# Optimization experiments

Measured on AMD Instinct MI355X. Metric: run time of the kernel, lower is better.

Reference implementation:

```python
import jax, jax.numpy as jnp
import numpy as np

N = 50000          # num graph nodes
E = 800000         # edges per direction
NGRAM, ODIM = 4, 32
DIMS = [128, 128, 64]
CLASSES = 128
MAXPE = 10
L2_EPS = 1e-12


def setup_inputs() -> dict:
    key = jax.random.key(0)
    ks = iter(jax.random.split(key, 40))
    d = {}
    d['x'] = jax.random.normal(next(ks), (N, DIMS[0]), jnp.float32)
    d['edge_index_in'] = jax.random.randint(next(ks), (2, E), 0, N, dtype=jnp.int64)
    d['edge_weight_in'] = jax.random.uniform(next(ks), (E,), jnp.float32)
    d['edge_index_out'] = jax.random.randint(next(ks), (2, E), 0, N, dtype=jnp.int64)
    d['edge_weight_out'] = jax.random.uniform(next(ks), (E,), jnp.float32)
    d['pe_table'] = jax.random.normal(next(ks), (MAXPE, ODIM), jnp.float32) * 0.05
    # per-layer DirectGCNLayer params (weights stored [in,out], i.e. torch W.T)
    for l in range(2):
        di, do = DIMS[l], DIMS[l + 1]
        s = 1.0 / np.sqrt(di)
        d[f'W_main_in_{l}'] = jax.random.normal(next(ks), (di, do), jnp.float32) * s
        d[f'W_main_out_{l}'] = jax.random.normal(next(ks), (di, do), jnp.float32) * s
        d[f'W_shared_{l}'] = jax.random.normal(next(ks), (di, do), jnp.float32) * s
        d[f'b_main_in_{l}'] = jnp.zeros((do,), jnp.float32)
        d[f'b_main_out_{l}'] = jnp.zeros((do,), jnp.float32)
        d[f'b_shared_in_{l}'] = jnp.zeros((do,), jnp.float32)
        d[f'b_shared_out_{l}'] = jnp.zeros((do,), jnp.float32)
        d[f'C_in_{l}'] = jnp.ones((N, 1), jnp.float32)
        d[f'C_out_{l}'] = jnp.ones((N, 1), jnp.float32)
    # residual projection for layer 1 (128 -> 64); layer 0 is identity
    d['res_W_1'] = jax.random.normal(next(ks), (DIMS[1], DIMS[2]), jnp.float32) * (1.0 / np.sqrt(DIMS[1]))
    d['res_b_1'] = jnp.zeros((DIMS[2],), jnp.float32)
    d['dec_W'] = jax.random.normal(next(ks), (DIMS[2], CLASSES), jnp.float32) * (1.0 / np.sqrt(DIMS[2]))
    d['dec_b'] = jnp.zeros((CLASSES,), jnp.float32)
    return d


def _prop(xW, ei, ew):
    # gather source, scale by edge weight, scatter-add to target (PyG aggr='add')
    return jax.ops.segment_sum(ew[:, None] * xW[ei[0]], ei[1], num_segments=N)


def _layer(h, ei_in, ew_in, ei_out, ew_out,
           Wmi, Wmo, Ws, bmi, bmo, bsi, bso, cin, cout):
    xs = h @ Ws  # shared transform, propagated over both edge sets
    ic = _prop(h @ Wmi, ei_in, ew_in) + bmi + _prop(xs, ei_in, ew_in) + bsi
    oc = _prop(h @ Wmo, ei_out, ew_out) + bmo + _prop(xs, ei_out, ew_out) + bso
    return cin * ic + cout * oc


def reference(x, edge_index_in, edge_weight_in, edge_index_out, edge_weight_out,
              pe_table,
              W_main_in_0, W_main_out_0, W_shared_0, b_main_in_0, b_main_out_0,
              b_shared_in_0, b_shared_out_0, C_in_0, C_out_0,
              W_main_in_1, W_main_out_1, W_shared_1, b_main_in_1, b_main_out_1,
              b_shared_in_1, b_shared_out_1, C_in_1, C_out_1,
              res_W_1, res_b_1, dec_W, dec_b):
    # positional encoding: add pe[:n_gram_len] to each n-gram slot
    h = (x.reshape(N, NGRAM, ODIM) + pe_table[:NGRAM][None]).reshape(N, NGRAM * ODIM)
    # layer 0 (identity residual); dropout p=0 / eval -> no-op
    h = jnp.tanh(_layer(h, edge_index_in, edge_weight_in, edge_index_out, edge_weight_out,
                        W_main_in_0, W_main_out_0, W_shared_0, b_main_in_0, b_main_out_0,
                        b_shared_in_0, b_shared_out_0, C_in_0, C_out_0) + h)
    # layer 1 (linear residual projection 128 -> 64)
    h = jnp.tanh(_layer(h, edge_index_in, edge_weight_in, edge_index_out, edge_weight_out,
                        W_main_in_1, W_main_out_1, W_shared_1, b_main_in_1, b_main_out_1,
                        b_shared_in_1, b_shared_out_1, C_in_1, C_out_1)
                 + h @ res_W_1 + res_b_1)
    logits = h @ dec_W + dec_b
    logp = jax.nn.log_softmax(logits, axis=-1)
    emb = h / (jnp.linalg.norm(h, axis=1, keepdims=True) + L2_EPS)
    return logp, emb
```

## Files before the change

### kernel.cpp

```cpp
#include <hip/hip_runtime.h>
#include <hip/hip_bf16.h>
#include <math.h>

typedef __hip_bfloat16  bf16;
typedef __hip_bfloat162 bf162;
typedef __attribute__((ext_vector_type(8))) short short8;
typedef __attribute__((ext_vector_type(4))) float floatx4;

#define BSZ     128
#define NBMAX   512
#define PACHUNK 8192

__device__ inline float4 bf4_to_f4(uint2 v) {
  float2 lo = __bfloat1622float2(*(bf162*)&v.x);
  float2 hi = __bfloat1622float2(*(bf162*)&v.y);
  return make_float4(lo.x, lo.y, hi.x, hi.y);
}
__device__ inline uint2 f4_to_bf4(float4 v) {
  bf162 lo = __float22bfloat162_rn(make_float2(v.x, v.y));
  bf162 hi = __float22bfloat162_rn(make_float2(v.z, v.w));
  uint2 r;
  r.x = *(unsigned*)&lo;
  r.y = *(unsigned*)&hi;
  return r;
}

__global__ __launch_bounds__(256) void k_bhist(const int* __restrict__ eiIn, const int* __restrict__ eiOut,
                                               int E, int* __restrict__ bcnt, int NB) {
  __shared__ int h[NBMAX];
  const int t = threadIdx.x;
  const int set = blockIdx.y;
  const int* dst = (set ? eiOut : eiIn) + E;
  for (int i = t; i < NB; i += 256) h[i] = 0;
  __syncthreads();
  const int base = blockIdx.x * PACHUNK;
  const int m = min(PACHUNK, E - base);
  #pragma unroll 4
  for (int r = 0; r < PACHUNK / 256; ++r) {
    int i = r * 256 + t;
    if (i < m) atomicAdd(&h[dst[base + i] >> 7], 1);
  }
  __syncthreads();
  for (int i = t; i < NB; i += 256) {
    int c = h[i];
    if (c) atomicAdd(&bcnt[set * NBMAX + i], c);
  }
}

__global__ __launch_bounds__(64) void k_bscan(const int* __restrict__ bcnt,
                                              int* __restrict__ BO, int* __restrict__ bcur, int NB) {
  const int set = blockIdx.x;
  const int t = threadIdx.x;
  int carry = 0;
  for (int base = 0; base < NB; base += 64) {
    int idx = base + t;
    int v = (idx < NB) ? bcnt[set * NBMAX + idx] : 0;
    int incl = v;
    #pragma unroll
    for (int d = 1; d < 64; d <<= 1) {
      int u = __shfl_up(incl, d, 64);
      if (t >= d) incl += u;
    }
    if (idx < NB) {
      int e = carry + incl - v;
      BO[set * NBMAX + idx]   = e;
      bcur[set * NBMAX + idx] = e;
    }
    carry += __shfl(incl, 63, 64);
  }
}

__global__ __launch_bounds__(256) void k_partA(const int* __restrict__ eiIn, const float* __restrict__ ewIn,
                                               const int* __restrict__ eiOut, const float* __restrict__ ewOut,
                                               int E, int* __restrict__ bucketCur,
                                               int2* __restrict__ sI, int2* __restrict__ sO, int NB) {
  __shared__ int2 staged[PACHUNK];
  __shared__ int cnt[NBMAX];
  __shared__ int sb[NBMAX];
  const int t = threadIdx.x;
  const int set = blockIdx.y;
  const int*   ei = set ? eiOut : eiIn;
  const float* ew = set ? ewOut : ewIn;
  int2* stg  = set ? sO : sI;
  int*  bcur = bucketCur + set * NBMAX;
  const int base = blockIdx.x * PACHUNK;
  const int m = min(PACHUNK, E - base);
  for (int b = t; b < NB; b += 256) cnt[b] = 0;
  __syncthreads();
  #pragma unroll 4
  for (int r = 0; r < PACHUNK / 256; ++r) {
    int i = r * 256 + t;
    if (i < m) atomicAdd(&cnt[ei[E + base + i] >> 7], 1);
  }
  __syncthreads();
  if (t < 64) {
    int carry = 0;
    int nch = (NB + 63) >> 6;
    for (int c = 0; c < nch; ++c) {
      int idx = c * 64 + t;
      int v = (idx < NB) ? cnt[idx] : 0;
      int incl = v;
      #pragma unroll
      for (int d = 1; d < 64; d <<= 1) {
        int u = __shfl_up(incl, d, 64);
        if (t >= d) incl += u;
      }
      if (idx < NB) sb[idx] = carry + incl - v;
      carry += __shfl(incl, 63, 64);
    }
  }
  __syncthreads();
  for (int b = t; b < NB; b += 256) {
    int c = cnt[b];
    if (c > 0) cnt[b] = atomicAdd(&bcur[b], c) - sb[b];
  }
  __syncthreads();
  #pragma unroll 4
  for (int r = 0; r < PACHUNK / 256; ++r) {
    int i = r * 256 + t;
    if (i < m) {
      int src = ei[base + i];
      int dst = ei[E + base + i];
      float w = ew[base + i];
      int b = dst >> 7;
      int rank = atomicAdd(&sb[b], 1);
      staged[rank] = make_int2(src | ((dst & 127) << 16) | (b << 23), __float_as_int(w));
    }
  }
  __syncthreads();
  #pragma unroll 4
  for (int r = 0; r < PACHUNK / 256; ++r) {
    int j = r * 256 + t;
    if (j < m) {
      int2 p = staged[j];
      int b = ((unsigned)p.x) >> 23;
      stg[cnt[b] + j] = p;
    }
  }
}

__global__ __launch_bounds__(256) void k_partB(const int* __restrict__ BO, const int* __restrict__ bcur,
                                               const int2* __restrict__ sI, const int2* __restrict__ sO,
                                               int2* __restrict__ eI, int2* __restrict__ eO,
                                               int* __restrict__ offsI, int* __restrict__ offsO, int N) {
  __shared__ int cnt[BSZ];
  __shared__ int excl[BSZ];
  __shared__ int cur[BSZ];
  const int t = threadIdx.x;
  const int b = blockIdx.x;
  const int set = blockIdx.y;
  const int2* stg = set ? sO : sI;
  int2* out = set ? eO : eI;
  int*  offs = set ? offsO : offsI;
  const int nlo = b << 7;
  const int nodes = min(BSZ, N - nlo);
  const int lo = BO[set * NBMAX + b];
  const int hi = bcur[set * NBMAX + b];
  if (t < BSZ) cnt[t] = 0;
  __syncthreads();
  for (int i = lo + t; i < hi; i += 256) atomicAdd(&cnt[(stg[i].x >> 16) & 127], 1);
  __syncthreads();
  if (t < 64) {
    int v0 = cnt[t];
    int i0 = v0;
    #pragma unroll
    for (int d = 1; d < 64; d <<= 1) { int u = __shfl_up(i0, d, 64); if (t >= d) i0 += u; }
    int v1 = cnt[64 + t];
    int i1 = v1;
    #pragma unroll
    for (int d = 1; d < 64; d <<= 1) { int u = __shfl_up(i1, d, 64); if (t >= d) i1 += u; }
    int tot0 = __shfl(i0, 63, 64);
    excl[t]      = i0 - v0;
    excl[64 + t] = tot0 + i1 - v1;
  }
  __syncthreads();
  if (t < BSZ) cur[t] = lo + excl[t];
  if (t < nodes) offs[nlo + t] = lo + excl[t];
  if (b == gridDim.x - 1 && t == 0) offs[N] = hi;
  __syncthreads();
  for (int i = lo + t; i < hi; i += 256) {
    int2 p = stg[i];
    int dl = (p.x >> 16) & 127;
    int pos = atomicAdd(&cur[dl], 1);
    out[pos] = make_int2(p.x & 0xffff, p.y);
  }
}

__global__ void k_wprep(const float* __restrict__ Wmi0, const float* __restrict__ Wmo0, const float* __restrict__ Ws0,
                        const float* __restrict__ Wmi1, const float* __restrict__ Wmo1, const float* __restrict__ Ws1,
                        const float* __restrict__ resW,
                        const float* __restrict__ bmi0, const float* __restrict__ bsi0,
                        const float* __restrict__ bmo0, const float* __restrict__ bso0,
                        const float* __restrict__ bmi1, const float* __restrict__ bsi1,
                        const float* __restrict__ bmo1, const float* __restrict__ bso1,
                        float* __restrict__ Wstack0, float* __restrict__ Wcat1,
                        float* __restrict__ bi0, float* __restrict__ bo0,
                        float* __restrict__ bi1, float* __restrict__ bo1) {
  int i = blockIdx.x * blockDim.x + threadIdx.x;
  if (i < 128 * 128) {
    Wstack0[i]             = Wmi0[i] + Ws0[i];
    Wstack0[128 * 128 + i] = Wmo0[i] + Ws0[i];
  }
  if (i < 128 * 192) {
    int k = i / 192, n = i % 192;
    float v;
    if (n < 64)       v = Wmi1[k * 64 + n]       + Ws1[k * 64 + n];
    else if (n < 128) v = Wmo1[k * 64 + n - 64]  + Ws1[k * 64 + n - 64];
    else              v = resW[k * 64 + n - 128];
    Wcat1[k * 192 + n] = v;
  }
  if (i < 128) { bi0[i] = bmi0[i] + bsi0[i]; bo0[i] = bmo0[i] + bso0[i]; }
  if (i < 64)  { bi1[i] = bmi1[i] + bsi1[i]; bo1[i] = bmo1[i] + bso1[i]; }
}

__device__ inline void pack_one(const float* __restrict__ W, bf16* __restrict__ P,
                                int id, int NT, int DO) {
  int lane = id & 63;
  int tile = id >> 6;
  int nt = tile % NT, kt = tile / NT;
  int col  = nt * 16 + (lane & 15);
  int krow = kt * 32 + (lane >> 4) * 8;
  bf16* dst = P + (size_t)id * 8;
  #pragma unroll
  for (int j = 0; j < 8; ++j) dst[j] = __float2bfloat16(W[(size_t)(krow + j) * DO + col]);
}
__global__ void k_packall(const float* __restrict__ W0, const float* __restrict__ W1,
                          const float* __restrict__ Wd,
                          bf16* __restrict__ P0, bf16* __restrict__ P1, bf16* __restrict__ Pd) {
  int id = blockIdx.x * blockDim.x + threadIdx.x;
  const int T0 = 8 * 8 * 64;
  const int T1 = 4 * 12 * 64;
  const int Td = 2 * 8 * 64;
  if (id < T0)                pack_one(W0, P0, id, 8, 128);
  else if (id < T0 + T1)      pack_one(W1, P1, id - T0, 12, 192);
  else if (id < T0 + T1 + Td) pack_one(Wd, Pd, id - T0 - T1, 8, 128);
}

__global__ void k_prep0(const float* __restrict__ x, const float* __restrict__ pe,
                        bf16* __restrict__ h0, int total) {
  int i = blockIdx.x * blockDim.x + threadIdx.x;
  if (i < total) h0[i] = __float2bfloat16(x[i] + pe[i & 127]);
}

__global__ __launch_bounds__(256) void k_agg0(const bf16* __restrict__ tb,
                                              const int* __restrict__ offsI, const int2* __restrict__ eI,
                                              const int* __restrict__ offsO, const int2* __restrict__ eO,
                                              const float* __restrict__ cin, const float* __restrict__ cou,
                                              bf16* __restrict__ aggC, int N) {
  int n = (blockIdx.x * blockDim.x + threadIdx.x) >> 6;
  int lane = threadIdx.x & 63;
  if (n >= N) return;
  const int dir = lane >> 5;
  const int sub = (lane >> 4) & 1;
  const int sl  = lane & 15;
  const int*   offs = dir ? offsO : offsI;
  const int2*  el   = dir ? eO : eI;
  const float* cc   = dir ? cou : cin;
  const char* base = (const char*)tb + sl * 16;
  float a0 = 0, a1 = 0, a2 = 0, a3 = 0, a4 = 0, a5 = 0, a6 = 0, a7 = 0;
  const int s0 = offs[n], s1 = offs[n + 1];
  int i = s0 + sub;
  for (; i + 6 < s1; i += 8) {
    int2 eA = el[i], eB = el[i + 2], eC = el[i + 4], eD = el[i + 6];
    uint4 vA = *(const uint4*)(base + ((size_t)(unsigned)eA.x << 8));
    uint4 vB = *(const uint4*)(base + ((size_t)(unsigned)eB.x << 8));
    uint4 vC = *(const uint4*)(base + ((size_t)(unsigned)eC.x << 8));
    uint4 vD = *(const uint4*)(base + ((size_t)(unsigned)eD.x << 8));
    float wA = __int_as_float(eA.y), wB = __int_as_float(eB.y);
    float wC = __int_as_float(eC.y), wD = __int_as_float(eD.y);
    float4 Al = bf4_to_f4(make_uint2(vA.x, vA.y)), Ah = bf4_to_f4(make_uint2(vA.z, vA.w));
    float4 Bl = bf4_to_f4(make_uint2(vB.x, vB.y)), Bh = bf4_to_f4(make_uint2(vB.z, vB.w));
    float4 Cl = bf4_to_f4(make_uint2(vC.x, vC.y)), Ch = bf4_to_f4(make_uint2(vC.z, vC.w));
    float4 Dl = bf4_to_f4(make_uint2(vD.x, vD.y)), Dh = bf4_to_f4(make_uint2(vD.z, vD.w));
    a0 += wA * Al.x + wB * Bl.x + wC * Cl.x + wD * Dl.x;
    a1 += wA * Al.y + wB * Bl.y + wC * Cl.y + wD * Dl.y;
    a2 += wA * Al.z + wB * Bl.z + wC * Cl.z + wD * Dl.z;
    a3 += wA * Al.w + wB * Bl.w + wC * Cl.w + wD * Dl.w;
    a4 += wA * Ah.x + wB * Bh.x + wC * Ch.x + wD * Dh.x;
    a5 += wA * Ah.y + wB * Bh.y + wC * Ch.y + wD * Dh.y;
    a6 += wA * Ah.z + wB * Bh.z + wC * Ch.z + wD * Dh.z;
    a7 += wA * Ah.w + wB * Bh.w + wC * Ch.w + wD * Dh.w;
  }
  for (; i < s1; i += 2) {
    int2 e = el[i];
    uint4 v = *(const uint4*)(base + ((size_t)(unsigned)e.x << 8));
    float w = __int_as_float(e.y);
    float4 lo = bf4_to_f4(make_uint2(v.x, v.y)), hi = bf4_to_f4(make_uint2(v.z, v.w));
    a0 += w * lo.x; a1 += w * lo.y; a2 += w * lo.z; a3 += w * lo.w;
    a4 += w * hi.x; a5 += w * hi.y; a6 += w * hi.z; a7 += w * hi.w;
  }
  a0 += __shfl_xor(a0, 16, 64); a1 += __shfl_xor(a1, 16, 64);
  a2 += __shfl_xor(a2, 16, 64); a3 += __shfl_xor(a3, 16, 64);
  a4 += __shfl_xor(a4, 16, 64); a5 += __shfl_xor(a5, 16, 64);
  a6 += __shfl_xor(a6, 16, 64); a7 += __shfl_xor(a7, 16, 64);
  if (sub == 0) {
    float c = cc[n];
    uint2 plo = f4_to_bf4(make_float4(c * a0, c * a1, c * a2, c * a3));
    uint2 phi = f4_to_bf4(make_float4(c * a4, c * a5, c * a6, c * a7));
    *(uint4*)(aggC + (size_t)n * 256 + dir * 128 + sl * 8) = make_uint4(plo.x, plo.y, phi.x, phi.y);
  }
}

__global__ __launch_bounds__(256) void k_mf0(const bf16* __restrict__ A,
                                             const bf16* __restrict__ Wp,
                                             const float* __restrict__ bi, const float* __restrict__ bo,
                                             const float* __restrict__ cin, const float* __restrict__ cou,
                                             const bf16* __restrict__ h0,
                                             bf16* __restrict__ h1, int N) {
  const int lane = threadIdx.x & 63;
  const int quad = lane >> 4, lc = lane & 15;
  const int bmw = blockIdx.x * 64 + (threadIdx.x >> 6) * 16;
  const int rowc = min(bmw + lc, N - 1);
  const bf16* ap = A + (size_t)rowc * 256 + quad * 8;
  const short8* bp = (const short8*)Wp + lane;
  floatx4 acc[8] = {};
  #pragma unroll
  for (int kt = 0; kt < 8; ++kt) {
    short8 af = *(const short8*)(ap + kt * 32);
    #pragma unroll
    for (int nt = 0; nt < 8; ++nt) {
      short8 bfr = bp[(kt * 8 + nt) * 64];
      acc[nt] = __builtin_amdgcn_mfma_f32_16x16x32_bf16(af, bfr, acc[nt], 0, 0, 0);
    }
  }
  float bif[8], bof[8];
  #pragma unroll
  for (int nt = 0; nt < 8; ++nt) {
    bif[nt] = bi[nt * 16 + lc];
    bof[nt] = bo[nt * 16 + lc];
  }
  #pragma unroll
  for (int r = 0; r < 4; ++r) {
    int gm = bmw + quad * 4 + r;
    if (gm < N) {
      float ci = cin[gm], co = cou[gm];
      #pragma unroll
      for (int nt = 0; nt < 8; ++nt) {
        int col = nt * 16 + lc;
        float v = acc[nt][r] + ci * bif[nt] + co * bof[nt]
                + __bfloat162float(h0[(size_t)gm * 128 + col]);
        h1[(size_t)gm * 128 + col] = __float2bfloat16(tanhf(v));
      }
    }
  }
}

__global__ __launch_bounds__(256) void k_mf1(const bf16* __restrict__ A,
                                             const bf16* __restrict__ Wp,
                                             bf16* __restrict__ t1g, bf16* __restrict__ t1r, int N) {
  const int lane = threadIdx.x & 63;
  const int quad = lane >> 4, lc = lane & 15;
  const int bmw = blockIdx.x * 64 + (threadIdx.x >> 6) * 16;
  const int rowc = min(bmw + lc, N - 1);
  const bf16* ap = A + (size_t)rowc * 128 + quad * 8;
  const short8* bp = (const short8*)Wp + lane;
  floatx4 acc[12] = {};
  #pragma unroll
  for (int kt = 0; kt < 4; ++kt) {
    short8 af = *(const short8*)(ap + kt * 32);
    #pragma unroll
    for (int nt = 0; nt < 12; ++nt) {
      short8 bfr = bp[(kt * 12 + nt) * 64];
      acc[nt] = __builtin_amdgcn_mfma_f32_16x16x32_bf16(af, bfr, acc[nt], 0, 0, 0);
    }
  }
  #pragma unroll
  for (int r = 0; r < 4; ++r) {
    int gm = bmw + quad * 4 + r;
    if (gm < N) {
      #pragma unroll
      for (int nt = 0; nt < 12; ++nt) {
        int col = nt * 16 + lc;
        bf16 v = __float2bfloat16(acc[nt][r]);
        if (col < 128) t1g[(size_t)gm * 128 + col]        = v;
        else           t1r[(size_t)gm * 64 + (col - 128)] = v;
      }
    }
  }
}

__global__ __launch_bounds__(256) void k_agg1(const bf16* __restrict__ t1g, const bf16* __restrict__ t1r,
                                              const int* __restrict__ offsI, const int2* __restrict__ eI,
                                              const int* __restrict__ offsO, const int2* __restrict__ eO,
                                              const float* __restrict__ bi, const float* __restrict__ bo,
                                              const float* __restrict__ resb,
                                              const float* __restrict__ cin, const float* __restrict__ cou,
                                              bf16* __restrict__ h2b, float* __restrict__ emb, int N) {
  int n = (blockIdx.x * blockDim.x + threadIdx.x) >> 6;
  int lane = threadIdx.x & 63;
  if (n >= N) return;
  const int sub = lane >> 4;
  const int sl  = lane & 15;
  const char* baseI = (const char*)t1g + sl * 8;
  const char* baseO = baseI + 128;
  float i0 = 0, i1 = 0, i2 = 0, i3 = 0, o0 = 0, o1 = 0, o2 = 0, o3 = 0;
  {
    int s0 = offsI[n], s1 = offsI[n + 1];
    int i = s0 + sub;
    for (; i + 4 < s1; i += 8) {
      int2 eA = eI[i], eB = eI[i + 4];
      float4 vA = bf4_to_f4(*(const uint2*)(baseI + ((size_t)(unsigned)eA.x << 8)));
      float4 vB = bf4_to_f4(*(const uint2*)(baseI + ((size_t)(unsigned)eB.x << 8)));
      float wA = __int_as_float(eA.y), wB = __int_as_float(eB.y);
      i0 += wA * vA.x + wB * vB.x;
      i1 += wA * vA.y + wB * vB.y;
      i2 += wA * vA.z + wB * vB.z;
      i3 += wA * vA.w + wB * vB.w;
    }
    for (; i < s1; i += 4) {
      int2 e = eI[i];
      float4 v = bf4_to_f4(*(const uint2*)(baseI + ((size_t)(unsigned)e.x << 8)));
      float w = __int_as_float(e.y);
      i0 += w * v.x; i1 += w * v.y; i2 += w * v.z; i3 += w * v.w;
    }
  }
  {
    int s0 = offsO[n], s1 = offsO[n + 1];
    int i = s0 + sub;
    for (; i + 4 < s1; i += 8) {
      int2 eA = eO[i], eB = eO[i + 4];
      float4 vA = bf4_to_f4(*(const uint2*)(baseO + ((size_t)(unsigned)eA.x << 8)));
      float4 vB = bf4_to_f4(*(const uint2*)(baseO + ((size_t)(unsigned)eB.x << 8)));
      float wA = __int_as_float(eA.y), wB = __int_as_float(eB.y);
      o0 += wA * vA.x + wB * vB.x;
      o1 += wA * vA.y + wB * vB.y;
      o2 += wA * vA.z + wB * vB.z;
      o3 += wA * vA.w + wB * vB.w;
    }
    for (; i < s1; i += 4) {
      int2 e = eO[i];
      float4 v = bf4_to_f4(*(const uint2*)(baseO + ((size_t)(unsigned)e.x << 8)));
      float w = __int_as_float(e.y);
      o0 += w * v.x; o1 += w * v.y; o2 += w * v.z; o3 += w * v.w;
    }
  }
  i0 += __shfl_xor(i0, 32, 64); i1 += __shfl_xor(i1, 32, 64);
  i2 += __shfl_xor(i2, 32, 64); i3 += __shfl_xor(i3, 32, 64);
  o0 += __shfl_xor(o0, 32, 64); o1 += __shfl_xor(o1, 32, 64);
  o2 += __shfl_xor(o2, 32, 64); o3 += __shfl_xor(o3, 32, 64);
  i0 += __shfl_xor(i0, 16, 64); i1 += __shfl_xor(i1, 16, 64);
  i2 += __shfl_xor(i2, 16, 64); i3 += __shfl_xor(i3, 16, 64);
  o0 += __shfl_xor(o0, 16, 64); o1 += __shfl_xor(o1, 16, 64);
  o2 += __shfl_xor(o2, 16, 64); o3 += __shfl_xor(o3, 16, 64);
  if (sub == 0) {
    const int c = sl * 4;
    float ci = cin[n], co = cou[n];
    float4 bif = *(const float4*)(bi + c);
    float4 bof = *(const float4*)(bo + c);
    float4 rbf = *(const float4*)(resb + c);
    float4 rv  = bf4_to_f4(*(const uint2*)((const char*)t1r + (size_t)n * 128 + sl * 8));
    float4 v;
    v.x = tanhf(ci * (i0 + bif.x) + co * (o0 + bof.x) + rv.x + rbf.x);
    v.y = tanhf(ci * (i1 + bif.y) + co * (o1 + bof.y) + rv.y + rbf.y);
    v.z = tanhf(ci * (i2 + bif.z) + co * (o2 + bof.z) + rv.z + rbf.z);
    v.w = tanhf(ci * (i3 + bif.w) + co * (o3 + bof.w) + rv.w + rbf.w);
    *(uint2*)(h2b + (size_t)n * 64 + c) = f4_to_bf4(v);
    float q = v.x * v.x + v.y * v.y + v.z * v.z + v.w * v.w;
    #pragma unroll
    for (int d = 1; d < 16; d <<= 1) q += __shfl_xor(q, d, 64);
    float inv = 1.0f / (sqrtf(q) + 1e-12f);
    *(float4*)(emb + (size_t)n * 64 + c) = make_float4(v.x * inv, v.y * inv, v.z * inv, v.w * inv);
  }
}

__global__ __launch_bounds__(256) void k_mfd(const bf16* __restrict__ A,
                                             const bf16* __restrict__ Wp,
                                             const float* __restrict__ bd,
                                             float* __restrict__ logp, int N) {
  const int lane = threadIdx.x & 63;
  const int quad = lane >> 4, lc = lane & 15;
  const int bmw = blockIdx.x * 64 + (threadIdx.x >> 6) * 16;
  const int rowc = min(bmw + lc, N - 1);
  const bf16* ap = A + (size_t)rowc * 64 + quad * 8;
  const short8* bp = (const short8*)Wp + lane;
  floatx4 acc[8] = {};
  #pragma unroll
  for (int kt = 0; kt < 2; ++kt) {
    short8 af = *(const short8*)(ap + kt * 32);
    #pragma unroll
    for (int nt = 0; nt < 8; ++nt) {
      short8 bfr = bp[(kt * 8 + nt) * 64];
      acc[nt] = __builtin_amdgcn_mfma_f32_16x16x32_bf16(af, bfr, acc[nt], 0, 0, 0);
    }
  }
  float bdv[8];
  #pragma unroll
  for (int nt = 0; nt < 8; ++nt) bdv[nt] = bd[nt * 16 + lc];
  #pragma unroll
  for (int r = 0; r < 4; ++r) {
    int gm = bmw + quad * 4 + r;
    float v[8];
    #pragma unroll
    for (int nt = 0; nt < 8; ++nt) v[nt] = acc[nt][r] + bdv[nt];
    float m = v[0];
    #pragma unroll
    for (int nt = 1; nt < 8; ++nt) m = fmaxf(m, v[nt]);
    #pragma unroll
    for (int d = 1; d < 16; d <<= 1) m = fmaxf(m, __shfl_xor(m, d, 64));
    float s = 0.f;
    #pragma unroll
    for (int nt = 0; nt < 8; ++nt) s += __expf(v[nt] - m);
    #pragma unroll
    for (int d = 1; d < 16; d <<= 1) s += __shfl_xor(s, d, 64);
    float lse = m + __logf(s);
    if (gm < N) {
      #pragma unroll
      for (int nt = 0; nt < 8; ++nt) logp[(size_t)gm * 128 + nt * 16 + lc] = v[nt] - lse;
    }
  }
}

extern "C" void kernel_launch(void* const* d_in, const int* in_sizes, int n_in,
                              void* d_out, int out_size, void* d_ws, size_t ws_size,
                              hipStream_t stream) {
  const float* x     = (const float*)d_in[0];
  const int*   ei_in = (const int*)d_in[1];
  const float* ew_in = (const float*)d_in[2];
  const int*   ei_ou = (const int*)d_in[3];
  const float* ew_ou = (const float*)d_in[4];
  const float* pe    = (const float*)d_in[5];
  const float* Wmi0  = (const float*)d_in[6];
  const float* Wmo0  = (const float*)d_in[7];
  const float* Wsh0  = (const float*)d_in[8];
  const float* bmi0  = (const float*)d_in[9];
  const float* bmo0  = (const float*)d_in[10];
  const float* bsi0  = (const float*)d_in[11];
  const float* bso0  = (const float*)d_in[12];
  const float* cin0  = (const float*)d_in[13];
  const float* cou0  = (const float*)d_in[14];
  const float* Wmi1  = (const float*)d_in[15];
  const float* Wmo1  = (const float*)d_in[16];
  const float* Wsh1  = (const float*)d_in[17];
  const float* bmi1  = (const float*)d_in[18];
  const float* bmo1  = (const float*)d_in[19];
  const float* bsi1  = (const float*)d_in[20];
  const float* bso1  = (const float*)d_in[21];
  const float* cin1  = (const float*)d_in[22];
  const float* cou1  = (const float*)d_in[23];
  const float* resW  = (const float*)d_in[24];
  const float* resb  = (const float*)d_in[25];
  const float* Wd    = (const float*)d_in[26];
  const float* bd    = (const float*)d_in[27];

  const int N = in_sizes[0] / 128;
  const int E = in_sizes[2];
  const int NB = (N + BSZ - 1) >> 7;

  char* ws = (char*)d_ws;
  size_t off = 0;
  auto alloc = [&](size_t bytes) -> char* {
    off = (off + 255) & ~(size_t)255;
    char* p = ws + off;
    off += bytes;
    return p;
  };
  bf16*  h0bf  = (bf16*)alloc((size_t)N * 128 * 2);
  bf16*  h1bf  = (bf16*)alloc((size_t)N * 128 * 2);
  bf16*  aggC  = (bf16*)alloc((size_t)N * 256 * 2);
  bf16*  h2b   = (bf16*)alloc((size_t)N * 64 * 2);
  float* Wst0  = (float*)alloc(256 * 128 * 4);
  float* Wcat1 = (float*)alloc(128 * 192 * 4);
  bf16*  Wp0   = (bf16*)alloc(256 * 128 * 2);
  bf16*  Wp1   = (bf16*)alloc(128 * 192 * 2);
  bf16*  Wpd   = (bf16*)alloc(64 * 128 * 2);
  float* bi0   = (float*)alloc(128 * 4);
  float* bo0   = (float*)alloc(128 * 4);
  float* bi1   = (float*)alloc(64 * 4);
  float* bo1   = (float*)alloc(64 * 4);
  int*   bcnt  = (int*)alloc((size_t)2 * NBMAX * 4);
  int*   BO    = (int*)alloc((size_t)2 * NBMAX * 4);
  int*   bcur  = (int*)alloc((size_t)2 * NBMAX * 4);
  int*   offsI = (int*)alloc((size_t)(N + 1) * 4);
  int*   offsO = (int*)alloc((size_t)(N + 1) * 4);
  int2*  sI    = (int2*)alloc((size_t)E * 8);
  int2*  sO    = (int2*)alloc((size_t)E * 8);
  int2*  eI    = (int2*)alloc((size_t)E * 8);
  int2*  eO    = (int2*)alloc((size_t)E * 8);
  bf16* t1g = aggC;
  bf16* t1r = t1g + (size_t)N * 128;

  (void)hipMemsetAsync(bcnt, 0, (size_t)2 * NBMAX * 4, stream);

  dim3 gc((E + PACHUNK - 1) / PACHUNK, 2);
  k_bhist<<<gc, 256, 0, stream>>>(ei_in, ei_ou, E, bcnt, NB);
  k_bscan<<<2, 64, 0, stream>>>(bcnt, BO, bcur, NB);
  k_partA<<<gc, 256, 0, stream>>>(ei_in, ew_in, ei_ou, ew_ou, E, bcur, sI, sO, NB);
  dim3 gb(NB, 2);
  k_partB<<<gb, 256, 0, stream>>>(BO, bcur, sI, sO, eI, eO, offsI, offsO, N);
  k_wprep<<<(128 * 192 + 255) / 256, 256, 0, stream>>>(Wmi0, Wmo0, Wsh0, Wmi1, Wmo1, Wsh1, resW,
                                                       bmi0, bsi0, bmo0, bso0, bmi1, bsi1, bmo1, bso1,
                                                       Wst0, Wcat1, bi0, bo0, bi1, bo1);
  k_packall<<<(8192 + 255) / 256, 256, 0, stream>>>(Wst0, Wcat1, Wd, Wp0, Wp1, Wpd);
  k_prep0<<<(N * 128 + 255) / 256, 256, 0, stream>>>(x, pe, h0bf, N * 128);

  int ab = (N + 3) / 4;
  int mb = (N + 63) / 64;
  k_agg0<<<ab, 256, 0, stream>>>(h0bf, offsI, eI, offsO, eO, cin0, cou0, aggC, N);
  k_mf0<<<mb, 256, 0, stream>>>(aggC, Wp0, bi0, bo0, cin0, cou0, h0bf, h1bf, N);
  k_mf1<<<mb, 256, 0, stream>>>(h1bf, Wp1, t1g, t1r, N);

  float* logp = (float*)d_out;
  float* emb  = logp + (size_t)N * 128;
  k_agg1<<<ab, 256, 0, stream>>>(t1g, t1r, offsI, eI, offsO, eO, bi1, bo1, resb, cin1, cou1,
                                 h2b, emb, N);
  k_mfd<<<mb, 256, 0, stream>>>(h2b, Wpd, bd, logp, N);
}
```

Measured before the change: 359.8 us.

## Split agg1 lanes by edge direction, deepen agg0 unroll, use nontemporal edge loads

k_agg1 now gives each half-wavefront one edge direction, with 8 lanes covering a row through 16-byte loads and 4 edges in flight per step, instead of walking both directions one after the other. The epilogue divides the h2b store and the normalized emb store between the two halves. k_agg0 gains a 16-edge unrolled loop, and both kernels read edge records as nontemporal 64-bit loads. The aim is more memory-level parallelism in the gather, at the cost of extra registers; the node index is now masked to 16 bits, which is only correct while N stays below 65536.

After: 385.5 us. +7.1%, slower.

```diff
diff --git a/kernel.cpp b/kernel.cpp
--- a/kernel.cpp
+++ b/kernel.cpp
@@ -6,6 +6,7 @@
 typedef __hip_bfloat162 bf162;
 typedef __attribute__((ext_vector_type(8))) short short8;
 typedef __attribute__((ext_vector_type(4))) float floatx4;
+typedef long long i64;
 
 #define BSZ     128
 #define NBMAX   512
@@ -260,14 +261,55 @@
   float a0 = 0, a1 = 0, a2 = 0, a3 = 0, a4 = 0, a5 = 0, a6 = 0, a7 = 0;
   const int s0 = offs[n], s1 = offs[n + 1];
   int i = s0 + sub;
+  for (; i + 14 < s1; i += 16) {
+    i64 pA = __builtin_nontemporal_load((const i64*)(el + i));
+    i64 pB = __builtin_nontemporal_load((const i64*)(el + i + 2));
+    i64 pC = __builtin_nontemporal_load((const i64*)(el + i + 4));
+    i64 pD = __builtin_nontemporal_load((const i64*)(el + i + 6));
+    i64 pE = __builtin_nontemporal_load((const i64*)(el + i + 8));
+    i64 pF = __builtin_nontemporal_load((const i64*)(el + i + 10));
+    i64 pG = __builtin_nontemporal_load((const i64*)(el + i + 12));
+    i64 pH = __builtin_nontemporal_load((const i64*)(el + i + 14));
+    uint4 vA = *(const uint4*)(base + ((size_t)(unsigned)(pA & 0xffff) << 8));
+    uint4 vB = *(const uint4*)(base + ((size_t)(unsigned)(pB & 0xffff) << 8));
+    uint4 vC = *(const uint4*)(base + ((size_t)(unsigned)(pC & 0xffff) << 8));
+    uint4 vD = *(const uint4*)(base + ((size_t)(unsigned)(pD & 0xffff) << 8));
+    uint4 vE = *(const uint4*)(base + ((size_t)(unsigned)(pE & 0xffff) << 8));
+    uint4 vF = *(const uint4*)(base + ((size_t)(unsigned)(pF & 0xffff) << 8));
+    uint4 vG = *(const uint4*)(base + ((size_t)(unsigned)(pG & 0xffff) << 8));
+    uint4 vH = *(const uint4*)(base + ((size_t)(unsigned)(pH & 0xffff) << 8));
+    float wA = __int_as_float((int)(pA >> 32)), wB = __int_as_float((int)(pB >> 32));
+    float wC = __int_as_float((int)(pC >> 32)), wD = __int_as_float((int)(pD >> 32));
+    float wE = __int_as_float((int)(pE >> 32)), wF = __int_as_float((int)(pF >> 32));
+    float wG = __int_as_float((int)(pG >> 32)), wH = __int_as_float((int)(pH >> 32));
+    float4 Al = bf4_to_f4(make_uint2(vA.x, vA.y)), Ah = bf4_to_f4(make_uint2(vA.z, vA.w));
+    float4 Bl = bf4_to_f4(make_uint2(vB.x, vB.y)), Bh = bf4_to_f4(make_uint2(vB.z, vB.w));
+    float4 Cl = bf4_to_f4(make_uint2(vC.x, vC.y)), Ch = bf4_to_f4(make_uint2(vC.z, vC.w));
+    float4 Dl = bf4_to_f4(make_uint2(vD.x, vD.y)), Dh = bf4_to_f4(make_uint2(vD.z, vD.w));
+    float4 El = bf4_to_f4(make_uint2(vE.x, vE.y)), Eh = bf4_to_f4(make_uint2(vE.z, vE.w));
+    float4 Fl = bf4_to_f4(make_uint2(vF.x, vF.y)), Fh = bf4_to_f4(make_uint2(vF.z, vF.w));
+    float4 Gl = bf4_to_f4(make_uint2(vG.x, vG.y)), Gh = bf4_to_f4(make_uint2(vG.z, vG.w));
+    float4 Hl = bf4_to_f4(make_uint2(vH.x, vH.y)), Hh = bf4_to_f4(make_uint2(vH.z, vH.w));
+    a0 += wA * Al.x + wB * Bl.x + wC * Cl.x + wD * Dl.x + wE * El.x + wF * Fl.x + wG * Gl.x + wH * Hl.x;
+    a1 += wA * Al.y + wB * Bl.y + wC * Cl.y + wD * Dl.y + wE * El.y + wF * Fl.y + wG * Gl.y + wH * Hl.y;
+    a2 += wA * Al.z + wB * Bl.z + wC * Cl.z + wD * Dl.z + wE * El.z + wF * Fl.z + wG * Gl.z + wH * Hl.z;
+    a3 += wA * Al.w + wB * Bl.w + wC * Cl.w + wD * Dl.w + wE * El.w + wF * Fl.w + wG * Gl.w + wH * Hl.w;
+    a4 += wA * Ah.x + wB * Bh.x + wC * Ch.x + wD * Dh.x + wE * Eh.x + wF * Fh.x + wG * Gh.x + wH * Hh.x;
+    a5 += wA * Ah.y + wB * Bh.y + wC * Ch.y + wD * Dh.y + wE * Eh.y + wF * Fh.y + wG * Gh.y + wH * Hh.y;
+    a6 += wA * Ah.z + wB * Bh.z + wC * Ch.z + wD * Dh.z + wE * Eh.z + wF * Fh.z + wG * Gh.z + wH * Hh.z;
+    a7 += wA * Ah.w + wB * Bh.w + wC * Ch.w + wD * Dh.w + wE * Eh.w + wF * Fh.w + wG * Gh.w + wH * Hh.w;
+  }
   for (; i + 6 < s1; i += 8) {
-    int2 eA = el[i], eB = el[i + 2], eC = el[i + 4], eD = el[i + 6];
-    uint4 vA = *(const uint4*)(base + ((size_t)(unsigned)eA.x << 8));
-    uint4 vB = *(const uint4*)(base + ((size_t)(unsigned)eB.x << 8));
-    uint4 vC = *(const uint4*)(base + ((size_t)(unsigned)eC.x << 8));
-    uint4 vD = *(const uint4*)(base + ((size_t)(unsigned)eD.x << 8));
-    float wA = __int_as_float(eA.y), wB = __int_as_float(eB.y);
-    float wC = __int_as_float(eC.y), wD = __int_as_float(eD.y);
+    i64 pA = __builtin_nontemporal_load((const i64*)(el + i));
+    i64 pB = __builtin_nontemporal_load((const i64*)(el + i + 2));
+    i64 pC = __builtin_nontemporal_load((const i64*)(el + i + 4));
+    i64 pD = __builtin_nontemporal_load((const i64*)(el + i + 6));
+    uint4 vA = *(const uint4*)(base + ((size_t)(unsigned)(pA & 0xffff) << 8));
+    uint4 vB = *(const uint4*)(base + ((size_t)(unsigned)(pB & 0xffff) << 8));
+    uint4 vC = *(const uint4*)(base + ((size_t)(unsigned)(pC & 0xffff) << 8));
+    uint4 vD = *(const uint4*)(base + ((size_t)(unsigned)(pD & 0xffff) << 8));
+    float wA = __int_as_float((int)(pA >> 32)), wB = __int_as_float((int)(pB >> 32));
+    float wC = __int_as_float((int)(pC >> 32)), wD = __int_as_float((int)(pD >> 32));
     float4 Al = bf4_to_f4(make_uint2(vA.x, vA.y)), Ah = bf4_to_f4(make_uint2(vA.z, vA.w));
     float4 Bl = bf4_to_f4(make_uint2(vB.x, vB.y)), Bh = bf4_to_f4(make_uint2(vB.z, vB.w));
     float4 Cl = bf4_to_f4(make_uint2(vC.x, vC.y)), Ch = bf4_to_f4(make_uint2(vC.z, vC.w));
@@ -282,9 +324,9 @@
     a7 += wA * Ah.w + wB * Bh.w + wC * Ch.w + wD * Dh.w;
   }
   for (; i < s1; i += 2) {
-    int2 e = el[i];
-    uint4 v = *(const uint4*)(base + ((size_t)(unsigned)e.x << 8));
-    float w = __int_as_float(e.y);
+    i64 p = __builtin_nontemporal_load((const i64*)(el + i));
+    uint4 v = *(const uint4*)(base + ((size_t)(unsigned)(p & 0xffff) << 8));
+    float w = __int_as_float((int)(p >> 32));
     float4 lo = bf4_to_f4(make_uint2(v.x, v.y)), hi = bf4_to_f4(make_uint2(v.z, v.w));
     a0 += w * lo.x; a1 += w * lo.y; a2 += w * lo.z; a3 += w * lo.w;
     a4 += w * hi.x; a5 += w * hi.y; a6 += w * hi.z; a7 += w * hi.w;
@@ -389,77 +431,95 @@
   int n = (blockIdx.x * blockDim.x + threadIdx.x) >> 6;
   int lane = threadIdx.x & 63;
   if (n >= N) return;
-  const int sub = lane >> 4;
-  const int sl  = lane & 15;
-  const char* baseI = (const char*)t1g + sl * 8;
-  const char* baseO = baseI + 128;
-  float i0 = 0, i1 = 0, i2 = 0, i3 = 0, o0 = 0, o1 = 0, o2 = 0, o3 = 0;
-  {
-    int s0 = offsI[n], s1 = offsI[n + 1];
-    int i = s0 + sub;
-    for (; i + 4 < s1; i += 8) {
-      int2 eA = eI[i], eB = eI[i + 4];
-      float4 vA = bf4_to_f4(*(const uint2*)(baseI + ((size_t)(unsigned)eA.x << 8)));
-      float4 vB = bf4_to_f4(*(const uint2*)(baseI + ((size_t)(unsigned)eB.x << 8)));
-      float wA = __int_as_float(eA.y), wB = __int_as_float(eB.y);
-      i0 += wA * vA.x + wB * vB.x;
-      i1 += wA * vA.y + wB * vB.y;
-      i2 += wA * vA.z + wB * vB.z;
-      i3 += wA * vA.w + wB * vB.w;
-    }
-    for (; i < s1; i += 4) {
-      int2 e = eI[i];
-      float4 v = bf4_to_f4(*(const uint2*)(baseI + ((size_t)(unsigned)e.x << 8)));
-      float w = __int_as_float(e.y);
-      i0 += w * v.x; i1 += w * v.y; i2 += w * v.z; i3 += w * v.w;
-    }
-  }
-  {
-    int s0 = offsO[n], s1 = offsO[n + 1];
-    int i = s0 + sub;
-    for (; i + 4 < s1; i += 8) {
-      int2 eA = eO[i], eB = eO[i + 4];
-      float4 vA = bf4_to_f4(*(const uint2*)(baseO + ((size_t)(unsigned)eA.x << 8)));
-      float4 vB = bf4_to_f4(*(const uint2*)(baseO + ((size_t)(unsigned)eB.x << 8)));
-      float wA = __int_as_float(eA.y), wB = __int_as_float(eB.y);
-      o0 += wA * vA.x + wB * vB.x;
-      o1 += wA * vA.y + wB * vB.y;
-      o2 += wA * vA.z + wB * vB.z;
-      o3 += wA * vA.w + wB * vB.w;
-    }
-    for (; i < s1; i += 4) {
-      int2 e = eO[i];
-      float4 v = bf4_to_f4(*(const uint2*)(baseO + ((size_t)(unsigned)e.x << 8)));
-      float w = __int_as_float(e.y);
-      o0 += w * v.x; o1 += w * v.y; o2 += w * v.z; o3 += w * v.w;
-    }
-  }
-  i0 += __shfl_xor(i0, 32, 64); i1 += __shfl_xor(i1, 32, 64);
-  i2 += __shfl_xor(i2, 32, 64); i3 += __shfl_xor(i3, 32, 64);
-  o0 += __shfl_xor(o0, 32, 64); o1 += __shfl_xor(o1, 32, 64);
-  o2 += __shfl_xor(o2, 32, 64); o3 += __shfl_xor(o3, 32, 64);
-  i0 += __shfl_xor(i0, 16, 64); i1 += __shfl_xor(i1, 16, 64);
-  i2 += __shfl_xor(i2, 16, 64); i3 += __shfl_xor(i3, 16, 64);
-  o0 += __shfl_xor(o0, 16, 64); o1 += __shfl_xor(o1, 16, 64);
-  o2 += __shfl_xor(o2, 16, 64); o3 += __shfl_xor(o3, 16, 64);
+  const int dir = lane >> 5;
+  const int sub = (lane >> 3) & 3;
+  const int sl  = lane & 7;
+  const int*   offs = dir ? offsO : offsI;
+  const int2*  el   = dir ? eO : eI;
+  const char* base = (const char*)t1g + dir * 128 + sl * 16;
+  float a0 = 0, a1 = 0, a2 = 0, a3 = 0, a4 = 0, a5 = 0, a6 = 0, a7 = 0;
+  const int s0 = offs[n], s1 = offs[n + 1];
+  int i = s0 + sub;
+  for (; i + 12 < s1; i += 16) {
+    i64 pA = __builtin_nontemporal_load((const i64*)(el + i));
+    i64 pB = __builtin_nontemporal_load((const i64*)(el + i + 4));
+    i64 pC = __builtin_nontemporal_load((const i64*)(el + i + 8));
+    i64 pD = __builtin_nontemporal_load((const i64*)(el + i + 12));
+    uint4 vA = *(const uint4*)(base + ((size_t)(unsigned)(pA & 0xffff) << 8));
+    uint4 vB = *(const uint4*)(base + ((size_t)(unsigned)(pB & 0xffff) << 8));
+    uint4 vC = *(const uint4*)(base + ((size_t)(unsigned)(pC & 0xffff) << 8));
+    uint4 vD = *(const uint4*)(base + ((size_t)(unsigned)(pD & 0xffff) << 8));
+    float wA = __int_as_float((int)(pA >> 32)), wB = __int_as_float((int)(pB >> 32));
+    float wC = __int_as_float((int)(pC >> 32)), wD = __int_as_float((int)(pD >> 32));
+    float4 Al = bf4_to_f4(make_uint2(vA.x, vA.y)), Ah = bf4_to_f4(make_uint2(vA.z, vA.w));
+    float4 Bl = bf4_to_f4(make_uint2(vB.x, vB.y)), Bh = bf4_to_f4(make_uint2(vB.z, vB.w));
+    float4 Cl = bf4_to_f4(make_uint2(vC.x, vC.y)), Ch = bf4_to_f4(make_uint2(vC.z, vC.w));
+    float4 Dl = bf4_to_f4(make_uint2(vD.x, vD.y)), Dh = bf4_to_f4(make_uint2(vD.z, vD.w));
+    a0 += wA * Al.x + wB * Bl.x + wC * Cl.x + wD * Dl.x;
+    a1 += wA * Al.y + wB * Bl.y + wC * Cl.y + wD * Dl.y;
+    a2 += wA * Al.z + wB * Bl.z + wC * Cl.z + wD * Dl.z;
+    a3 += wA * Al.w + wB * Bl.w + wC * Cl.w + wD * Dl.w;
+    a4 += wA * Ah.x + wB * Bh.x + wC * Ch.x + wD * Dh.x;
+    a5 += wA * Ah.y + wB * Bh.y + wC * Ch.y + wD * Dh.y;
+    a6 += wA * Ah.z + wB * Bh.z + wC * Ch.z + wD * Dh.z;
+    a7 += wA * Ah.w + wB * Bh.w + wC * Ch.w + wD * Dh.w;
+  }
+  for (; i < s1; i += 4) {
+    i64 p = __builtin_nontemporal_load((const i64*)(el + i));
+    uint4 v = *(const uint4*)(base + ((size_t)(unsigned)(p & 0xffff) << 8));
+    float w = __int_as_float((int)(p >> 32));
+    float4 lo = bf4_to_f4(make_uint2(v.x, v.y)), hi = bf4_to_f4(make_uint2(v.z, v.w));
+    a0 += w * lo.x; a1 += w * lo.y; a2 += w * lo.z; a3 += w * lo.w;
+    a4 += w * hi.x; a5 += w * hi.y; a6 += w * hi.z; a7 += w * hi.w;
+  }
+  a0 += __shfl_xor(a0, 8, 64);  a1 += __shfl_xor(a1, 8, 64);
+  a2 += __shfl_xor(a2, 8, 64);  a3 += __shfl_xor(a3, 8, 64);
+  a4 += __shfl_xor(a4, 8, 64);  a5 += __shfl_xor(a5, 8, 64);
+  a6 += __shfl_xor(a6, 8, 64);  a7 += __shfl_xor(a7, 8, 64);
+  a0 += __shfl_xor(a0, 16, 64); a1 += __shfl_xor(a1, 16, 64);
+  a2 += __shfl_xor(a2, 16, 64); a3 += __shfl_xor(a3, 16, 64);
+  a4 += __shfl_xor(a4, 16, 64); a5 += __shfl_xor(a5, 16, 64);
+  a6 += __shfl_xor(a6, 16, 64); a7 += __shfl_xor(a7, 16, 64);
+  float b0 = __shfl_xor(a0, 32, 64), b1 = __shfl_xor(a1, 32, 64);
+  float b2 = __shfl_xor(a2, 32, 64), b3 = __shfl_xor(a3, 32, 64);
+  float b4 = __shfl_xor(a4, 32, 64), b5 = __shfl_xor(a5, 32, 64);
+  float b6 = __shfl_xor(a6, 32, 64), b7 = __shfl_xor(a7, 32, 64);
   if (sub == 0) {
-    const int c = sl * 4;
+    const int c = sl * 8;
     float ci = cin[n], co = cou[n];
-    float4 bif = *(const float4*)(bi + c);
-    float4 bof = *(const float4*)(bo + c);
-    float4 rbf = *(const float4*)(resb + c);
-    float4 rv  = bf4_to_f4(*(const uint2*)((const char*)t1r + (size_t)n * 128 + sl * 8));
-    float4 v;
-    v.x = tanhf(ci * (i0 + bif.x) + co * (o0 + bof.x) + rv.x + rbf.x);
-    v.y = tanhf(ci * (i1 + bif.y) + co * (o1 + bof.y) + rv.y + rbf.y);
-    v.z = tanhf(ci * (i2 + bif.z) + co * (o2 + bof.z) + rv.z + rbf.z);
-    v.w = tanhf(ci * (i3 + bif.w) + co * (o3 + bof.w) + rv.w + rbf.w);
-    *(uint2*)(h2b + (size_t)n * 64 + c) = f4_to_bf4(v);
-    float q = v.x * v.x + v.y * v.y + v.z * v.z + v.w * v.w;
-    #pragma unroll
-    for (int d = 1; d < 16; d <<= 1) q += __shfl_xor(q, d, 64);
-    float inv = 1.0f / (sqrtf(q) + 1e-12f);
-    *(float4*)(emb + (size_t)n * 64 + c) = make_float4(v.x * inv, v.y * inv, v.z * inv, v.w * inv);
+    float s_in[8]  = { dir ? b0 : a0, dir ? b1 : a1, dir ? b2 : a2, dir ? b3 : a3,
+                       dir ? b4 : a4, dir ? b5 : a5, dir ? b6 : a6, dir ? b7 : a7 };
+    float s_ou[8]  = { dir ? a0 : b0, dir ? a1 : b1, dir ? a2 : b2, dir ? a3 : b3,
+                       dir ? a4 : b4, dir ? a5 : b5, dir ? a6 : b6, dir ? a7 : b7 };
+    float4 bif0 = *(const float4*)(bi + c),   bif1 = *(const float4*)(bi + c + 4);
+    float4 bof0 = *(const float4*)(bo + c),   bof1 = *(const float4*)(bo + c + 4);
+    float4 rbf0 = *(const float4*)(resb + c), rbf1 = *(const float4*)(resb + c + 4);
+    uint4 rvu = *(const uint4*)((const char*)t1r + (size_t)n * 128 + sl * 16);
+    float4 rv0 = bf4_to_f4(make_uint2(rvu.x, rvu.y));
+    float4 rv1 = bf4_to_f4(make_uint2(rvu.z, rvu.w));
+    float bif[8] = { bif0.x, bif0.y, bif0.z, bif0.w, bif1.x, bif1.y, bif1.z, bif1.w };
+    float bof[8] = { bof0.x, bof0.y, bof0.z, bof0.w, bof1.x, bof1.y, bof1.z, bof1.w };
+    float rbf[8] = { rbf0.x, rbf0.y, rbf0.z, rbf0.w, rbf1.x, rbf1.y, rbf1.z, rbf1.w };
+    float rvf[8] = { rv0.x, rv0.y, rv0.z, rv0.w, rv1.x, rv1.y, rv1.z, rv1.w };
+    float v[8];
+    float q = 0.f;
+    #pragma unroll
+    for (int k = 0; k < 8; ++k) {
+      v[k] = tanhf(ci * (s_in[k] + bif[k]) + co * (s_ou[k] + bof[k]) + rvf[k] + rbf[k]);
+      q += v[k] * v[k];
+    }
+    q += __shfl_xor(q, 1, 64);
+    q += __shfl_xor(q, 2, 64);
+    q += __shfl_xor(q, 4, 64);
+    if (dir == 0) {
+      uint2 plo = f4_to_bf4(make_float4(v[0], v[1], v[2], v[3]));
+      uint2 phi = f4_to_bf4(make_float4(v[4], v[5], v[6], v[7]));
+      *(uint4*)(h2b + (size_t)n * 64 + c) = make_uint4(plo.x, plo.y, phi.x, phi.y);
+    } else {
+      float inv = 1.0f / (sqrtf(q) + 1e-12f);
+      *(float4*)(emb + (size_t)n * 64 + c)     = make_float4(v[0] * inv, v[1] * inv, v[2] * inv, v[3] * inv);
+      *(float4*)(emb + (size_t)n * 64 + c + 4) = make_float4(v[4] * inv, v[5] * inv, v[6] * inv, v[7] * inv);
+    }
   }
 }
 
```
